# Performance work log

Hardware: AMD Instinct MI355X
Metric: run time of the kernel (lower is better)

Reference implementation:

```python
import jax, jax.numpy as jnp
import numpy as np

F = 1024
H = 16
DH = F // H  # 64
MLP = 4096
EPS = 1e-5


def layernorm(x, g, b):
    mu = x.mean(-1, keepdims=True)
    var = ((x - mu) ** 2).mean(-1, keepdims=True)
    return (x - mu) * jax.lax.rsqrt(var + EPS) * g + b


def softmax_off_by_one(a):
    e = jnp.exp(a - a.max(-1, keepdims=True))
    return e / (1.0 + e.sum(-1, keepdims=True))


def setup_inputs() -> dict:
    key = jax.random.key(0)
    ks = jax.random.split(key, 12)
    s = 0.02
    return {
        "x": jax.random.normal(ks[0], (2, 2048, F), jnp.float32),
        "ln1_g": jnp.ones((F,), jnp.float32),
        "ln1_b": jnp.zeros((F,), jnp.float32),
        "Wq": jax.random.normal(ks[1], (F, F), jnp.float32) * s,
        "bq": jnp.zeros((F,), jnp.float32),
        "Wk": jax.random.normal(ks[2], (F, F), jnp.float32) * s,
        "bk": jnp.zeros((F,), jnp.float32),
        "Wv": jax.random.normal(ks[3], (F, F), jnp.float32) * s,
        "bv": jnp.zeros((F,), jnp.float32),
        "Wo": jax.random.normal(ks[4], (F, F), jnp.float32) * s,
        "bo": jnp.zeros((F,), jnp.float32),
        "slim": jnp.ones((H,), jnp.float32),
        "ln2_g": jnp.ones((F,), jnp.float32),
        "ln2_b": jnp.zeros((F,), jnp.float32),
        "W1": jax.random.normal(ks[5], (F, MLP), jnp.float32) * s,
        "b1": jnp.zeros((MLP,), jnp.float32),
        "W2": jax.random.normal(ks[6], (MLP, F), jnp.float32) * s,
        "b2": jnp.zeros((F,), jnp.float32),
    }


def reference(x, ln1_g, ln1_b, Wq, bq, Wk, bk, Wv, bv, Wo, bo, slim,
              ln2_g, ln2_b, W1, b1, W2, b2):
    b, n, f = x.shape
    h = layernorm(x, ln1_g, ln1_b)
    # project and split heads: [b, H, n, DH]
    q = (h @ Wq + bq).reshape(b, n, H, DH).transpose(0, 2, 1, 3)
    k = (h @ Wk + bk).reshape(b, n, H, DH).transpose(0, 2, 1, 3)
    v = (h @ Wv + bv).reshape(b, n, H, DH).transpose(0, 2, 1, 3)
    att = jnp.einsum('bhid,bhjd->bhij', q, k) / (DH ** 0.5)
    probs = softmax_off_by_one(att)  # off-by-one softmax
    probs = probs * slim[None, :, None, None]  # slimming after softmax
    attn = jnp.einsum('bhij,bhjd->bihd', probs, v).reshape(b, n, F)
    out = attn @ Wo + bo + x  # residual 1
    h2 = layernorm(out, ln2_g, ln2_b)
    m = jax.nn.gelu(h2 @ W1 + b1, approximate=False)
    m = jax.nn.gelu(m @ W2 + b2, approximate=False)
    return m + out  # residual 2
```

## Files before the change

kernel.cpp:

```cpp
#include <hip/hip_runtime.h>
#include <hip/hip_bf16.h>

typedef __hip_bfloat16 bf16;
typedef short bf16x8 __attribute__((ext_vector_type(8)));
typedef float f32x4 __attribute__((ext_vector_type(4)));

__device__ __forceinline__ float gelu_f(float x) {
  return 0.5f * x * (1.f + erff(x * 0.70710678118654752f));
}

__device__ __forceinline__ unsigned short f2bfu(float f) {
  bf16 h = __float2bfloat16(f);
  unsigned short u;
  __builtin_memcpy(&u, &h, 2);
  return u;
}

__device__ __forceinline__ void load16_lds(const bf16* g, bf16* l) {
  __builtin_amdgcn_global_load_lds(
      (const __attribute__((address_space(1))) unsigned int*)g,
      (__attribute__((address_space(3))) unsigned int*)l, 16, 0, 0);
}

__global__ __launch_bounds__(256) void transpose_cast(
    const float* __restrict__ src, bf16* __restrict__ dst, int R, int C) {
  __shared__ float tile[32][33];
  int tx = threadIdx.x & 31, ty = threadIdx.x >> 5;
  int r0 = blockIdx.y * 32, c0 = blockIdx.x * 32;
  #pragma unroll
  for (int i = ty; i < 32; i += 8)
    tile[i][tx] = src[(size_t)(r0 + i) * C + (c0 + tx)];
  __syncthreads();
  #pragma unroll
  for (int i = ty; i < 32; i += 8)
    dst[(size_t)(c0 + i) * R + (r0 + tx)] = __float2bfloat16(tile[tx][i]);
}

__global__ __launch_bounds__(256) void ln_kernel(
    const float* __restrict__ x, const float* __restrict__ g,
    const float* __restrict__ b, bf16* __restrict__ y) {
  int row = blockIdx.x;
  int t = threadIdx.x;
  const float4* xr = (const float4*)(x + (size_t)row * 1024);
  float4 v = xr[t];
  float s = v.x + v.y + v.z + v.w;
  float ss = v.x * v.x + v.y * v.y + v.z * v.z + v.w * v.w;
  #pragma unroll
  for (int off = 32; off >= 1; off >>= 1) {
    s += __shfl_xor(s, off);
    ss += __shfl_xor(ss, off);
  }
  __shared__ float red[8];
  int wv = t >> 6;
  if ((t & 63) == 0) { red[wv] = s; red[4 + wv] = ss; }
  __syncthreads();
  float S = red[0] + red[1] + red[2] + red[3];
  float SS = red[4] + red[5] + red[6] + red[7];
  float mu = S * (1.f / 1024.f);
  float var = SS * (1.f / 1024.f) - mu * mu;
  float inv = rsqrtf(var + 1e-5f);
  float4 gv = ((const float4*)g)[t];
  float4 bv = ((const float4*)b)[t];
  ushort4 o;
  o.x = f2bfu((v.x - mu) * inv * gv.x + bv.x);
  o.y = f2bfu((v.y - mu) * inv * gv.y + bv.y);
  o.z = f2bfu((v.z - mu) * inv * gv.z + bv.z);
  o.w = f2bfu((v.w - mu) * inv * gv.w + bv.w);
  ((ushort4*)(y + (size_t)row * 1024))[t] = o;
}

template <int EPI>
__global__ __launch_bounds__(256) void gemm_bf16(
    const bf16* __restrict__ A, const bf16* __restrict__ Bt,
    const float* __restrict__ bias0, const float* __restrict__ bias1,
    const float* __restrict__ bias2, const float* __restrict__ resid,
    void* __restrict__ C0, void* __restrict__ C1, void* __restrict__ C2,
    int M, int N, int K) {
  __shared__ __align__(16) bf16 As[2][128 * 32];
  __shared__ __align__(16) bf16 Bs[2][128 * 32];
  const int t = threadIdx.x, lane = t & 63, w = t >> 6;
  const int wm = (w >> 1) * 64, wn = (w & 1) * 64;
  const int m0 = blockIdx.y * 128, n0 = blockIdx.x * 128;

  const int koff = (EPI == 6) ? (int)blockIdx.z * 1024 : 0;
  const int kc_len = (EPI == 6) ? 1024 : K;

  const int srow = lane >> 2;
  const int sgrp = lane & 3;
  f32x4 acc[4][4] = {};

  const bf16* Abase = A + (size_t)m0 * K + koff;
  const bf16* Bbase = Bt + (size_t)n0 * K + koff;

  auto stage = [&](int buf, int kt) {
    #pragma unroll
    for (int c = 0; c < 2; ++c) {
      int row = w * 32 + c * 16 + srow;
      int sw = (row & 3) ^ ((row >> 2) & 3);
      int gg = sgrp ^ sw;
      const bf16* ga = Abase + (size_t)row * K + kt + gg * 8;
      const bf16* gb = Bbase + (size_t)row * K + kt + gg * 8;
      load16_lds(ga, &As[buf][(w * 32 + c * 16) * 32]);
      load16_lds(gb, &Bs[buf][(w * 32 + c * 16) * 32]);
    }
  };

  const int q8 = (((lane >> 4) ^ (lane & 3) ^ ((lane >> 2) & 3))) * 8;
  const int fr = lane & 15;

  const int nk = kc_len >> 5;
  stage(0, 0);
  for (int i = 0; i < nk; ++i) {
    const int cur = i & 1;
    __syncthreads();
    if (i + 1 < nk) stage(cur ^ 1, (i + 1) << 5);
    bf16x8 af[4], bfr[4];
    #pragma unroll
    for (int mc = 0; mc < 4; ++mc)
      af[mc] = *(const bf16x8*)&As[cur][(wm + mc * 16 + fr) * 32 + q8];
    #pragma unroll
    for (int nc = 0; nc < 4; ++nc)
      bfr[nc] = *(const bf16x8*)&Bs[cur][(wn + nc * 16 + fr) * 32 + q8];
    #pragma unroll
    for (int mc = 0; mc < 4; ++mc)
      #pragma unroll
      for (int nc = 0; nc < 4; ++nc)
        acc[mc][nc] = __builtin_amdgcn_mfma_f32_16x16x32_bf16(
            af[mc], bfr[nc], acc[mc][nc], 0, 0, 0);
  }

  if constexpr (EPI == 0) {
    const int which = n0 >> 10;
    const float* bp = which == 0 ? bias0 : which == 1 ? bias1 : bias2;
    bf16* qk = (bf16*)(which == 0 ? C0 : C1);
    #pragma unroll
    for (int mc = 0; mc < 4; ++mc) {
      #pragma unroll
      for (int reg = 0; reg < 4; ++reg) {
        int m = m0 + wm + mc * 16 + ((lane >> 4) << 2) + reg;
        int b = m >> 11, tok = m & 2047;
        #pragma unroll
        for (int nc = 0; nc < 4; ++nc) {
          int n = n0 + wn + nc * 16 + (lane & 15);
          int nn = n & 1023, hh = nn >> 6, d = n & 63;
          float val = acc[mc][nc][reg] + bp[nn];
          if (which == 2)
            ((bf16*)C2)[(size_t)((b * 16 + hh) * 64 + d) * 2048 + tok] =
                __float2bfloat16(val);
          else
            qk[(size_t)((b * 16 + hh) * 2048 + tok) * 64 + d] =
                __float2bfloat16(val);
        }
      }
    }
  } else if constexpr (EPI == 6) {
    bf16* pout = (bf16*)C0 + (size_t)blockIdx.z * M * N;
    #pragma unroll
    for (int mc = 0; mc < 4; ++mc) {
      #pragma unroll
      for (int reg = 0; reg < 4; ++reg) {
        int m = m0 + wm + mc * 16 + ((lane >> 4) << 2) + reg;
        #pragma unroll
        for (int nc = 0; nc < 4; ++nc) {
          int n = n0 + wn + nc * 16 + (lane & 15);
          pout[(size_t)m * N + n] = __float2bfloat16(acc[mc][nc][reg]);
        }
      }
    }
  } else {
    #pragma unroll
    for (int mc = 0; mc < 4; ++mc) {
      #pragma unroll
      for (int reg = 0; reg < 4; ++reg) {
        int m = m0 + wm + mc * 16 + ((lane >> 4) << 2) + reg;
        #pragma unroll
        for (int nc = 0; nc < 4; ++nc) {
          int n = n0 + wn + nc * 16 + (lane & 15);
          float val = acc[mc][nc][reg] + bias0[n];
          size_t idx = (size_t)m * N + n;
          if constexpr (EPI == 3) {
            ((float*)C0)[idx] = val + resid[idx];
          } else if constexpr (EPI == 4) {
            ((bf16*)C0)[idx] = __float2bfloat16(gelu_f(val));
          } else {
            ((float*)C0)[idx] = gelu_f(val) + resid[idx];
          }
        }
      }
    }
  }
}

__global__ __launch_bounds__(256) void reduce_mlp2(
    const bf16* __restrict__ part, const float* __restrict__ b2,
    const float* __restrict__ out1, float* __restrict__ out) {
  const int row = blockIdx.x, t = threadIdx.x;
  const size_t base = (size_t)row * 1024 + t * 4;
  float sum[4] = {0.f, 0.f, 0.f, 0.f};
  #pragma unroll
  for (int kc = 0; kc < 4; ++kc) {
    ushort4 u = *(const ushort4*)(part + (size_t)kc * 4096 * 1024 + base);
    unsigned short us[4] = {u.x, u.y, u.z, u.w};
    #pragma unroll
    for (int j = 0; j < 4; ++j) {
      bf16 h;
      __builtin_memcpy(&h, &us[j], 2);
      sum[j] += __bfloat162float(h);
    }
  }
  float4 bv = ((const float4*)b2)[t];
  float4 rv = *(const float4*)(out1 + base);
  float4 o;
  o.x = gelu_f(sum[0] + bv.x) + rv.x;
  o.y = gelu_f(sum[1] + bv.y) + rv.y;
  o.z = gelu_f(sum[2] + bv.z) + rv.z;
  o.w = gelu_f(sum[3] + bv.w) + rv.w;
  *(float4*)(out + base) = o;
}

__global__ __launch_bounds__(256) void attn_kernel(
    const bf16* __restrict__ q, const bf16* __restrict__ k,
    const bf16* __restrict__ vt, const float* __restrict__ slim,
    bf16* __restrict__ attn) {
  __shared__ __align__(16) bf16 Ks[64][64];
  __shared__ __align__(16) bf16 Vs[64][64];
  __shared__ __align__(16) bf16 Ps[4][16][72];

  const int t = threadIdx.x, lane = t & 63, w = t >> 6;
  const int fr = lane & 15, qd = lane >> 4;
  const int bh = blockIdx.y;
  const int q0 = blockIdx.x * 64;
  const size_t bhbase = (size_t)bh * 2048 * 64;

  const int qrow = q0 + w * 16 + fr;
  const bf16* qp = q + bhbase + (size_t)qrow * 64 + qd * 8;
  bf16x8 qf0 = *(const bf16x8*)qp;
  bf16x8 qf1 = *(const bf16x8*)(qp + 32);

  const int srow = lane >> 3;
  const int sg = lane & 7;

  f32x4 o_acc[4] = {};
  float m_lane[4] = {-3.0e38f, -3.0e38f, -3.0e38f, -3.0e38f};
  float l_lane[4] = {0.f, 0.f, 0.f, 0.f};
  const float C = 0.18033688011f;

  for (int j0 = 0; j0 < 2048; j0 += 64) {
    __syncthreads();
    #pragma unroll
    for (int c = 0; c < 2; ++c) {
      int r = w * 16 + c * 8 + srow;
      int gk = sg ^ (r & 7);
      load16_lds(k + bhbase + (size_t)(j0 + r) * 64 + gk * 8, &Ks[w * 16 + c * 8][0]);
      load16_lds(vt + bhbase + (size_t)r * 2048 + j0 + gk * 8, &Vs[w * 16 + c * 8][0]);
    }
    __syncthreads();

    f32x4 z[4];
    #pragma unroll
    for (int nc = 0; nc < 4; ++nc) {
      int kr = nc * 16 + fr;
      bf16x8 kf0 = *(const bf16x8*)&Ks[kr][(qd ^ (kr & 7)) * 8];
      bf16x8 kf1 = *(const bf16x8*)&Ks[kr][((qd + 4) ^ (kr & 7)) * 8];
      f32x4 zz = {};
      zz = __builtin_amdgcn_mfma_f32_16x16x32_bf16(qf0, kf0, zz, 0, 0, 0);
      zz = __builtin_amdgcn_mfma_f32_16x16x32_bf16(qf1, kf1, zz, 0, 0, 0);
      z[nc] = zz;
    }

    #pragma unroll
    for (int nc = 0; nc < 4; ++nc)
      #pragma unroll
      for (int r = 0; r < 4; ++r) {
        float p = exp2f(z[nc][r] * C);
        l_lane[r] += p;
        m_lane[r] = fmaxf(m_lane[r], z[nc][r]);
        Ps[w][qd * 4 + r][nc * 16 + fr] = __float2bfloat16(p);
      }

    bf16x8 pf0 = *(const bf16x8*)&Ps[w][fr][qd * 8];
    bf16x8 pf1 = *(const bf16x8*)&Ps[w][fr][32 + qd * 8];
    #pragma unroll
    for (int dc = 0; dc < 4; ++dc) {
      int vr = dc * 16 + fr;
      bf16x8 vf0 = *(const bf16x8*)&Vs[vr][(qd ^ (vr & 7)) * 8];
      bf16x8 vf1 = *(const bf16x8*)&Vs[vr][((qd + 4) ^ (vr & 7)) * 8];
      o_acc[dc] = __builtin_amdgcn_mfma_f32_16x16x32_bf16(pf0, vf0, o_acc[dc], 0, 0, 0);
      o_acc[dc] = __builtin_amdgcn_mfma_f32_16x16x32_bf16(pf1, vf1, o_acc[dc], 0, 0, 0);
    }
  }

  #pragma unroll
  for (int off = 1; off <= 8; off <<= 1)
    #pragma unroll
    for (int r = 0; r < 4; ++r) {
      l_lane[r] += __shfl_xor(l_lane[r], off);
      m_lane[r] = fmaxf(m_lane[r], __shfl_xor(m_lane[r], off));
    }

  const int b = bh >> 4, hh = bh & 15;
  const float sl = slim[hh];
  #pragma unroll
  for (int r = 0; r < 4; ++r) {
    float inv = sl / (exp2f(m_lane[r] * C) + l_lane[r]);
    int mrow = b * 2048 + q0 + w * 16 + qd * 4 + r;
    #pragma unroll
    for (int dc = 0; dc < 4; ++dc) {
      int col = hh * 64 + dc * 16 + fr;
      attn[(size_t)mrow * 1024 + col] = __float2bfloat16(o_acc[dc][r] * inv);
    }
  }
}

extern "C" void kernel_launch(void* const* d_in, const int* in_sizes, int n_in,
                              void* d_out, int out_size, void* d_ws, size_t ws_size,
                              hipStream_t stream) {
  const float* x    = (const float*)d_in[0];
  const float* ln1g = (const float*)d_in[1];
  const float* ln1b = (const float*)d_in[2];
  const float* Wq   = (const float*)d_in[3];
  const float* bq   = (const float*)d_in[4];
  const float* Wk   = (const float*)d_in[5];
  const float* bk   = (const float*)d_in[6];
  const float* Wv   = (const float*)d_in[7];
  const float* bv   = (const float*)d_in[8];
  const float* Wo   = (const float*)d_in[9];
  const float* bo   = (const float*)d_in[10];
  const float* slim = (const float*)d_in[11];
  const float* ln2g = (const float*)d_in[12];
  const float* ln2b = (const float*)d_in[13];
  const float* W1   = (const float*)d_in[14];
  const float* b1   = (const float*)d_in[15];
  const float* W2   = (const float*)d_in[16];
  const float* b2   = (const float*)d_in[17];

  char* p = (char*)d_ws;
  auto take = [&](size_t nbytes) {
    char* r = p;
    p += (nbytes + 255) & ~(size_t)255;
    return r;
  };
  bf16* Wqkv_t = (bf16*)take((size_t)3072 * 1024 * 2);
  bf16* Wo_t = (bf16*)take((size_t)1024 * 1024 * 2);
  bf16* W1_t = (bf16*)take((size_t)4096 * 1024 * 2);
  bf16* W2_t = (bf16*)take((size_t)1024 * 4096 * 2);
  bf16* h1   = (bf16*)take((size_t)4096 * 1024 * 2);
  bf16* qb   = (bf16*)take((size_t)4096 * 1024 * 2);
  bf16* kb   = (bf16*)take((size_t)4096 * 1024 * 2);
  bf16* vtb  = (bf16*)take((size_t)4096 * 1024 * 2);
  bf16* attn = (bf16*)take((size_t)4096 * 1024 * 2);
  float* out1 = (float*)take((size_t)4096 * 1024 * 4);
  bf16* h2   = (bf16*)take((size_t)4096 * 1024 * 2);
  bf16* m1   = (bf16*)take((size_t)4096 * 4096 * 2);

  bf16* parts = h1;

  dim3 blk(256);

  transpose_cast<<<dim3(32, 32), blk, 0, stream>>>(Wq, Wqkv_t, 1024, 1024);
  transpose_cast<<<dim3(32, 32), blk, 0, stream>>>(Wk, Wqkv_t + (size_t)1024 * 1024, 1024, 1024);
  transpose_cast<<<dim3(32, 32), blk, 0, stream>>>(Wv, Wqkv_t + (size_t)2048 * 1024, 1024, 1024);
  transpose_cast<<<dim3(32, 32), blk, 0, stream>>>(Wo, Wo_t, 1024, 1024);
  transpose_cast<<<dim3(128, 32), blk, 0, stream>>>(W1, W1_t, 1024, 4096);
  transpose_cast<<<dim3(32, 128), blk, 0, stream>>>(W2, W2_t, 4096, 1024);

  ln_kernel<<<4096, blk, 0, stream>>>(x, ln1g, ln1b, h1);

  gemm_bf16<0><<<dim3(24, 32), blk, 0, stream>>>(
      h1, Wqkv_t, bq, bk, bv, nullptr, qb, kb, vtb, 4096, 3072, 1024);

  attn_kernel<<<dim3(32, 32), blk, 0, stream>>>(qb, kb, vtb, slim, attn);

  gemm_bf16<3><<<dim3(8, 32), blk, 0, stream>>>(
      attn, Wo_t, bo, nullptr, nullptr, x, out1, nullptr, nullptr, 4096, 1024, 1024);

  ln_kernel<<<4096, blk, 0, stream>>>(out1, ln2g, ln2b, h2);

  gemm_bf16<4><<<dim3(32, 32), blk, 0, stream>>>(
      h2, W1_t, b1, nullptr, nullptr, nullptr, m1, nullptr, nullptr, 4096, 4096, 1024);

  gemm_bf16<6><<<dim3(8, 32, 4), blk, 0, stream>>>(
      m1, W2_t, nullptr, nullptr, nullptr, nullptr, parts, nullptr, nullptr,
      4096, 1024, 4096);
  reduce_mlp2<<<4096, blk, 0, stream>>>(parts, b2, out1, (float*)d_out);
}
```

Before: 435.1 us.

## Double-buffer K/V tiles in attention and fold softmax scale into Q projection

The attention kernel now keeps two LDS buffers for the K and V tiles. It prefetches the next 64-key tile while computing on the current one, so each iteration needs one barrier instead of two and global-load latency can overlap with MFMA work. The 1/sqrt(d)·log2(e) scale is applied once in the QKV projection epilogue when Q is written, which removes a per-score multiply. The running max is now tracked on exp2 values, which is equivalent because the kernel never subtracts the max. Rounding Q to bf16 after scaling changes numerics slightly, and the second buffer doubles K/V LDS use, which may lower occupancy.

```diff
diff --git a/kernel.cpp b/kernel.cpp
--- a/kernel.cpp
+++ b/kernel.cpp
@@ -133,6 +133,7 @@
     const int which = n0 >> 10;
     const float* bp = which == 0 ? bias0 : which == 1 ? bias1 : bias2;
     bf16* qk = (bf16*)(which == 0 ? C0 : C1);
+    const float qscale = 0.18033688011112042f;
     #pragma unroll
     for (int mc = 0; mc < 4; ++mc) {
       #pragma unroll
@@ -147,6 +148,9 @@
           if (which == 2)
             ((bf16*)C2)[(size_t)((b * 16 + hh) * 64 + d) * 2048 + tok] =
                 __float2bfloat16(val);
+          else if (which == 0)
+            qk[(size_t)((b * 16 + hh) * 2048 + tok) * 64 + d] =
+                __float2bfloat16(val * qscale);
           else
             qk[(size_t)((b * 16 + hh) * 2048 + tok) * 64 + d] =
                 __float2bfloat16(val);
@@ -222,8 +226,8 @@
     const bf16* __restrict__ q, const bf16* __restrict__ k,
     const bf16* __restrict__ vt, const float* __restrict__ slim,
     bf16* __restrict__ attn) {
-  __shared__ __align__(16) bf16 Ks[64][64];
-  __shared__ __align__(16) bf16 Vs[64][64];
+  __shared__ __align__(16) bf16 Ks[2][64][64];
+  __shared__ __align__(16) bf16 Vs[2][64][64];
   __shared__ __align__(16) bf16 Ps[4][16][72];
 
   const int t = threadIdx.x, lane = t & 63, w = t >> 6;
@@ -241,27 +245,33 @@
   const int sg = lane & 7;
 
   f32x4 o_acc[4] = {};
-  float m_lane[4] = {-3.0e38f, -3.0e38f, -3.0e38f, -3.0e38f};
+  float m_lane[4] = {0.f, 0.f, 0.f, 0.f};
   float l_lane[4] = {0.f, 0.f, 0.f, 0.f};
-  const float C = 0.18033688011f;
-
-  for (int j0 = 0; j0 < 2048; j0 += 64) {
-    __syncthreads();
+
+  auto stage = [&](int buf, int j0) {
     #pragma unroll
     for (int c = 0; c < 2; ++c) {
       int r = w * 16 + c * 8 + srow;
       int gk = sg ^ (r & 7);
-      load16_lds(k + bhbase + (size_t)(j0 + r) * 64 + gk * 8, &Ks[w * 16 + c * 8][0]);
-      load16_lds(vt + bhbase + (size_t)r * 2048 + j0 + gk * 8, &Vs[w * 16 + c * 8][0]);
-    }
+      load16_lds(k + bhbase + (size_t)(j0 + r) * 64 + gk * 8,
+                 &Ks[buf][w * 16 + c * 8][0]);
+      load16_lds(vt + bhbase + (size_t)r * 2048 + j0 + gk * 8,
+                 &Vs[buf][w * 16 + c * 8][0]);
+    }
+  };
+
+  stage(0, 0);
+  for (int it = 0; it < 32; ++it) {
+    const int cur = it & 1;
     __syncthreads();
+    if (it + 1 < 32) stage(cur ^ 1, (it + 1) * 64);
 
     f32x4 z[4];
     #pragma unroll
     for (int nc = 0; nc < 4; ++nc) {
       int kr = nc * 16 + fr;
-      bf16x8 kf0 = *(const bf16x8*)&Ks[kr][(qd ^ (kr & 7)) * 8];
-      bf16x8 kf1 = *(const bf16x8*)&Ks[kr][((qd + 4) ^ (kr & 7)) * 8];
+      bf16x8 kf0 = *(const bf16x8*)&Ks[cur][kr][(qd ^ (kr & 7)) * 8];
+      bf16x8 kf1 = *(const bf16x8*)&Ks[cur][kr][((qd + 4) ^ (kr & 7)) * 8];
       f32x4 zz = {};
       zz = __builtin_amdgcn_mfma_f32_16x16x32_bf16(qf0, kf0, zz, 0, 0, 0);
       zz = __builtin_amdgcn_mfma_f32_16x16x32_bf16(qf1, kf1, zz, 0, 0, 0);
@@ -272,9 +282,9 @@
     for (int nc = 0; nc < 4; ++nc)
       #pragma unroll
       for (int r = 0; r < 4; ++r) {
-        float p = exp2f(z[nc][r] * C);
+        float p = exp2f(z[nc][r]);
         l_lane[r] += p;
-        m_lane[r] = fmaxf(m_lane[r], z[nc][r]);
+        m_lane[r] = fmaxf(m_lane[r], p);
         Ps[w][qd * 4 + r][nc * 16 + fr] = __float2bfloat16(p);
       }
 
@@ -283,8 +293,8 @@
     #pragma unroll
     for (int dc = 0; dc < 4; ++dc) {
       int vr = dc * 16 + fr;
-      bf16x8 vf0 = *(const bf16x8*)&Vs[vr][(qd ^ (vr & 7)) * 8];
-      bf16x8 vf1 = *(const bf16x8*)&Vs[vr][((qd + 4) ^ (vr & 7)) * 8];
+      bf16x8 vf0 = *(const bf16x8*)&Vs[cur][vr][(qd ^ (vr & 7)) * 8];
+      bf16x8 vf1 = *(const bf16x8*)&Vs[cur][vr][((qd + 4) ^ (vr & 7)) * 8];
       o_acc[dc] = __builtin_amdgcn_mfma_f32_16x16x32_bf16(pf0, vf0, o_acc[dc], 0, 0, 0);
       o_acc[dc] = __builtin_amdgcn_mfma_f32_16x16x32_bf16(pf1, vf1, o_acc[dc], 0, 0, 0);
     }
@@ -302,7 +312,7 @@
   const float sl = slim[hh];
   #pragma unroll
   for (int r = 0; r < 4; ++r) {
-    float inv = sl / (exp2f(m_lane[r] * C) + l_lane[r]);
+    float inv = sl / (m_lane[r] + l_lane[r]);
     int mrow = b * 2048 + q0 + w * 16 + qd * 4 + r;
     #pragma unroll
     for (int dc = 0; dc < 4; ++dc) {
```

After: 468.1 us. 1.08x slower.
